# Kernel tuning notes

Measured on AMD Instinct MI355X. Metric: run time of the kernel, lower is better.

## Reference

```python
import jax, jax.numpy as jnp
import numpy as np

H = 50   # hidden_dim (hardcoded in module)
D = 16   # input_dim
B = 4096
T = 512

def _uniform(key, shape, k):
    return jax.random.uniform(key, shape, jnp.float32, -k, k)

def setup_inputs() -> dict:
    key = jax.random.key(0)
    ks = jax.random.split(key, 12)
    k = 1.0 / np.sqrt(H)  # PyTorch LSTM/Linear init bound
    return {
        "x": jax.random.normal(ks[0], (B, T, D), jnp.float32),
        "W_ih0": _uniform(ks[1], (4 * H, D), k),
        "W_hh0": _uniform(ks[2], (4 * H, H), k),
        "b_ih0": _uniform(ks[3], (4 * H,), k),
        "b_hh0": _uniform(ks[4], (4 * H,), k),
        "W_ih1": _uniform(ks[5], (4 * H, H), k),
        "W_hh1": _uniform(ks[6], (4 * H, H), k),
        "b_ih1": _uniform(ks[7], (4 * H,), k),
        "b_hh1": _uniform(ks[8], (4 * H,), k),
        "W_fc": _uniform(ks[9], (1, H), k),
        "b_fc": _uniform(ks[10], (1,), k),
    }

def _lstm_layer(x_tbd, W_ih, W_hh, b):
    # x_tbd: [T, B, Din]; returns (ys [T,B,H], h_final [B,H])
    Bsz = x_tbd.shape[1]
    # precompute input projections for all timesteps: [T, B, 4H]
    xproj = jnp.einsum('tbd,gd->tbg', x_tbd, W_ih) + b

    def step(carry, xp):
        h, c = carry
        gates = xp + h @ W_hh.T  # [B, 4H]
        i, f, g, o = jnp.split(gates, 4, axis=-1)  # torch gate order i,f,g,o
        i = jax.nn.sigmoid(i)
        f = jax.nn.sigmoid(f)
        g = jnp.tanh(g)
        o = jax.nn.sigmoid(o)
        c = f * c + i * g
        h = o * jnp.tanh(c)
        return (h, c), h

    init = (jnp.zeros((Bsz, H), x_tbd.dtype), jnp.zeros((Bsz, H), x_tbd.dtype))
    (h_fin, _), ys = jax.lax.scan(step, init, xproj)
    return ys, h_fin

def reference(x, W_ih0, W_hh0, b_ih0, b_hh0, W_ih1, W_hh1, b_ih1, b_hh1, W_fc, b_fc):
    x_tbd = jnp.transpose(x, (1, 0, 2))  # [T, B, D]
    ys0, _ = _lstm_layer(x_tbd, W_ih0, W_hh0, b_ih0 + b_hh0)
    _, h_n = _lstm_layer(ys0, W_ih1, W_hh1, b_ih1 + b_hh1)
    return h_n @ W_fc.T + b_fc  # [B, 1]
```

## Files before the change

### kernel.cpp

```cpp
#include <hip/hip_runtime.h>


#define TSTEPS 512
#define DIN 16
#define HID 50
#define BPB 16

typedef _Float16 half8 __attribute__((ext_vector_type(8)));
typedef _Float16 half4v __attribute__((ext_vector_type(4)));
typedef float f32x4 __attribute__((ext_vector_type(4)));

#define MF(A, B, C) __builtin_amdgcn_mfma_f32_16x16x32_f16((A), (B), (C), 0, 0, 0)

#define HBUF 2304
#define XBUF 1280
#define H0_O 0
#define H1_O 4608
#define X_O  9216
#define SH_BYTES (9216 + 4 * XBUF)

#define BAR() asm volatile("s_waitcnt lgkmcnt(0)\ns_barrier" ::: "memory")

__device__ __forceinline__ unsigned pack2h(float a, float b) {
  union { _Float16 h[2]; unsigned u; } pk;
  pk.h[0] = (_Float16)a;
  pk.h[1] = (_Float16)b;
  return pk.u;
}

__device__ __forceinline__ void cell2(const f32x4 gA, const f32x4 gB,
                                      float& cA, float& cB, float& hA, float& hB) {
  const float L2E = 1.4426950408889634f;
  float eiA = __builtin_amdgcn_exp2f(-L2E * gA[0]);
  float efA = __builtin_amdgcn_exp2f(-L2E * gA[1]);
  float egA = __builtin_amdgcn_exp2f(fminf(2.f * L2E * gA[2], 40.f));
  float eoA = __builtin_amdgcn_exp2f(-L2E * gA[3]);
  float eiB = __builtin_amdgcn_exp2f(-L2E * gB[0]);
  float efB = __builtin_amdgcn_exp2f(-L2E * gB[1]);
  float egB = __builtin_amdgcn_exp2f(fminf(2.f * L2E * gB[2], 40.f));
  float eoB = __builtin_amdgcn_exp2f(-L2E * gB[3]);
  float aA = 1.f + eiA, fA = 1.f + efA, bA = 1.f + egA;
  float aB = 1.f + eiB, fB = 1.f + efB, bB = 1.f + egB;
  float abA = aA * bA, abB = aB * bB;
  float tA = fmaf(egA - 1.f, fA, cA * abA);
  float tB = fmaf(egB - 1.f, fB, cB * abB);
  cA = tA * __builtin_amdgcn_rcpf(fA * abA);
  cB = tB * __builtin_amdgcn_rcpf(fB * abB);
  float ecA = __builtin_amdgcn_exp2f(fminf(2.f * L2E * cA, 40.f));
  float ecB = __builtin_amdgcn_exp2f(fminf(2.f * L2E * cB, 40.f));
  float qA = (1.f + eoA) * (1.f + ecA);
  float qB = (1.f + eoB) * (1.f + ecB);
  float r2 = __builtin_amdgcn_rcpf(qA * qB);
  hA = (ecA - 1.f) * (r2 * qB);
  hB = (ecB - 1.f) * (r2 * qA);
}

__device__ __forceinline__ half8 load_wfrag(const float* __restrict__ W, int kld,
                                            bool permk, int kreal, int gt, int kt,
                                            int lane) {
  const int gp = 16 * gt + (lane & 15);
  const int u = gp >> 2, j = gp & 3;
  const int kb = kt * 32 + (lane >> 4) * 8;
  half8 f;
#pragma unroll
  for (int i = 0; i < 8; ++i) {
    const int p = kb + i;
    const int kk = permk ? ((p & ~7) + (((p & 1) << 2) | ((p >> 1) & 3))) : p;
    float v = (u < HID && kk < kreal) ? W[(j * HID + u) * kld + kk] : 0.f;
    f[i] = (_Float16)v;
  }
  return f;
}

extern "C" __global__ void __launch_bounds__(512, 2)
lstm2_v8(const float* __restrict__ x,
         const float* __restrict__ Wih0, const float* __restrict__ Whh0,
         const float* __restrict__ bih0, const float* __restrict__ bhh0,
         const float* __restrict__ Wih1, const float* __restrict__ Whh1,
         const float* __restrict__ bih1, const float* __restrict__ bhh1,
         const float* __restrict__ Wfc, const float* __restrict__ bfc,
         float* __restrict__ out) {
  __shared__ __align__(16) char sh[SH_BYTES];
  const int tid = threadIdx.x;
  const int lane = tid & 63;
  const int wv = tid >> 6;
  const int bcol = lane & 15;
  const int kg = lane >> 4;
  const int bbase = blockIdx.x * BPB;
  const bool comp = (wv < 7);

  const int sbb = lane >> 2, q = lane & 3;
  const float* xrow = x + ((size_t)(bbase + sbb) * TSTEPS) * DIN + q * 4;

  for (int i = tid; i < SH_BYTES / 4; i += 512) ((int*)sh)[i] = 0;

  half8 w0x[2], w0h[2][2], w1i[2][2], w1h[2][2];
  f32x4 bias0v[2] = {{0,0,0,0},{0,0,0,0}}, bias1v[2] = {{0,0,0,0},{0,0,0,0}};
  if (comp) {
#pragma unroll
    for (int gi = 0; gi < 2; ++gi) {
      const int gt = 2 * wv + gi;
      w0x[gi] = load_wfrag(Wih0, DIN, false, DIN, gt, 0, lane);
#pragma unroll
      for (int kt = 0; kt < 2; ++kt) {
        w0h[gi][kt] = load_wfrag(Whh0, HID, true, HID, gt, kt, lane);
        w1i[gi][kt] = load_wfrag(Wih1, HID, true, HID, gt, kt, lane);
        w1h[gi][kt] = load_wfrag(Whh1, HID, true, HID, gt, kt, lane);
      }
      const int u = 8 * wv + 4 * gi + kg;
      if (u < HID) {
#pragma unroll
        for (int j = 0; j < 4; ++j) {
          bias0v[gi][j] = bih0[j * HID + u] + bhh0[j * HID + u];
          bias1v[gi][j] = bih1[j * HID + u] + bhh1[j * HID + u];
        }
      }
    }
  }
  float c0[2] = {0.f, 0.f}, c1[2] = {0.f, 0.f};
  const int hoff = bcol * 144 + kg * 16;
  const int xoff = bcol * 80 + kg * 16;
  const int wo32 = bcol * 144 + wv * 16 + kg * 4;

  BAR();

  if (wv == 7) {
#pragma unroll
    for (int t = 0; t < 3; ++t) {
      float4 xq = *(const float4*)(xrow + (size_t)t * DIN);
      half4v h4;
#pragma unroll
      for (int i = 0; i < 4; ++i) h4[i] = (_Float16)((const float*)&xq)[i];
      *(half4v*)(sh + X_O + t * XBUF + sbb * 80 + q * 8) = h4;
    }
  }
  BAR();

  float4 xrA, xrB;
  half8 bxc;
  if (comp) {
    half8 bx0 = *(const half8*)(sh + X_O + 0 * XBUF + xoff);
    bxc = *(const half8*)(sh + X_O + 1 * XBUF + xoff);
    f32x4 a0 = MF(w0x[0], bx0, bias0v[0]);
    f32x4 a1 = MF(w0x[1], bx0, bias0v[1]);
    float h0a, h0b;
    cell2(a0, a1, c0[0], c0[1], h0a, h0b);
    *(unsigned*)(sh + H0_O + wo32) = pack2h(h0a, h0b);
  } else if (wv == 7) {
    xrA = *(const float4*)(xrow + (size_t)3 * DIN);
    xrB = *(const float4*)(xrow + (size_t)4 * DIN);
  }
  BAR();

#define STEPCOMP(P, XSN)                                                       \
  do {                                                                         \
    half8 bh0[2], bh1[2];                                                      \
    _Pragma("unroll") for (int kt = 0; kt < 2; ++kt) {                         \
      bh0[kt] = *(const half8*)(sh + H0_O + (P)*HBUF + hoff + kt * 64);        \
      bh1[kt] = *(const half8*)(sh + H1_O + (P)*HBUF + hoff + kt * 64);        \
    }                                                                          \
    half8 bxn = *(const half8*)(sh + X_O + (XSN)*XBUF + xoff);                 \
    float h1n[2], h0n[2];                                                      \
    _Pragma("unroll") for (int gi = 0; gi < 2; ++gi) {                         \
      f32x4 qv = MF(w1i[gi][0], bh0[0], bias1v[gi]);                           \
      qv = MF(w1h[gi][0], bh1[0], qv);                                         \
      qv = MF(w1i[gi][1], bh0[1], qv);                                         \
      qv = MF(w1h[gi][1], bh1[1], qv);                                         \
      f32x4 rv = MF(w0x[gi], bxc, bias0v[gi]);                                 \
      rv = MF(w0h[gi][0], bh0[0], rv);                                         \
      rv = MF(w0h[gi][1], bh0[1], rv);                                         \
      cell2(qv, rv, c1[gi], c0[gi], h1n[gi], h0n[gi]);                         \
    }                                                                          \
    *(unsigned*)(sh + H1_O + ((P) ^ 1) * HBUF + wo32) = pack2h(h1n[0], h1n[1]);\
    *(unsigned*)(sh + H0_O + ((P) ^ 1) * HBUF + wo32) = pack2h(h0n[0], h0n[1]);\
    bxc = bxn;                                                                 \
  } while (0)

#define STEPX(T, SLOT, XR)                                                     \
  do {                                                                         \
    half4v h4;                                                                 \
    _Pragma("unroll") for (int i = 0; i < 4; ++i)                              \
        h4[i] = (_Float16)((const float*)&(XR))[i];                            \
    *(half4v*)(sh + X_O + (SLOT)*XBUF + sbb * 80 + q * 8) = h4;                \
    int tl = (T) + 5;                                                          \
    if (tl > TSTEPS - 1) tl = TSTEPS - 1;                                      \
    (XR) = *(const float4*)(xrow + (size_t)tl * DIN);                          \
  } while (0)

  for (int s = 0; s < TSTEPS; s += 4) {
    if (comp) { STEPCOMP(0, 2); } else if (wv == 7) { STEPX(s, 3, xrA); }
    BAR();
    if (comp) { STEPCOMP(1, 3); } else if (wv == 7) { STEPX(s + 1, 0, xrB); }
    BAR();
    if (comp) { STEPCOMP(0, 0); } else if (wv == 7) { STEPX(s + 2, 1, xrA); }
    BAR();
    if (comp) { STEPCOMP(1, 1); } else if (wv == 7) { STEPX(s + 3, 2, xrB); }
    BAR();
  }

  if (tid < BPB) {
    float acc = bfc[0];
#pragma unroll 10
    for (int u = 0; u < HID; ++u) {
      const int pp = (u & ~7) + 2 * (u & 3) + ((u >> 2) & 1);
      float h = (float)(*(const _Float16*)(sh + H1_O + tid * 144 + pp * 2));
      acc = fmaf(Wfc[u], h, acc);
    }
    out[bbase + tid] = acc;
  }
}

extern "C" void kernel_launch(void* const* d_in, const int* in_sizes, int n_in,
                              void* d_out, int out_size, void* d_ws, size_t ws_size,
                              hipStream_t stream) {
  (void)in_sizes; (void)n_in; (void)d_ws; (void)ws_size; (void)out_size;
  lstm2_v8<<<dim3(4096 / BPB), dim3(512), 0, stream>>>(
      (const float*)d_in[0], (const float*)d_in[1], (const float*)d_in[2],
      (const float*)d_in[3], (const float*)d_in[4], (const float*)d_in[5],
      (const float*)d_in[6], (const float*)d_in[7], (const float*)d_in[8],
      (const float*)d_in[9], (const float*)d_in[10], (float*)d_out);
}
```

Before: 398.1 us.

## Fold exp2 scaling constants into weights/bias, pack cell math, reorder MFMA chains

Premultiplies the gate weights and biases by -log2(e) (or 2*log2(e) for the g gate) so the cell no longer multiplies before each exp2. The cell state is kept pre-scaled by 2*log2(e), which removes the multiply before the tanh(c) exponent. The cell math is rewritten over 2-wide float vectors to allow packed FP32 ops, and h is packed with cvt_pkrtz. The MFMA chains for the two gate tiles are interleaved, and the layer-0 cell is computed and stored before layer 1 to hide MFMA latency. The trade-off is different fp16 rounding of the scaled weights, round-toward-zero conversion, and changed clamping.

```diff
diff --git a/kernel.cpp b/kernel.cpp
--- a/kernel.cpp
+++ b/kernel.cpp
@@ -8,7 +8,9 @@
 
 typedef _Float16 half8 __attribute__((ext_vector_type(8)));
 typedef _Float16 half4v __attribute__((ext_vector_type(4)));
+typedef __fp16 fp16x2 __attribute__((ext_vector_type(2)));
 typedef float f32x4 __attribute__((ext_vector_type(4)));
+typedef float f32x2 __attribute__((ext_vector_type(2)));
 
 #define MF(A, B, C) __builtin_amdgcn_mfma_f32_16x16x32_f16((A), (B), (C), 0, 0, 0)
 
@@ -21,43 +23,49 @@
 
 #define BAR() asm volatile("s_waitcnt lgkmcnt(0)\ns_barrier" ::: "memory")
 
+#define NL2E  (-1.4426950408889634f)
+#define P2L2E (2.8853900817779268f)
+
 __device__ __forceinline__ unsigned pack2h(float a, float b) {
-  union { _Float16 h[2]; unsigned u; } pk;
-  pk.h[0] = (_Float16)a;
-  pk.h[1] = (_Float16)b;
+  union { fp16x2 h; unsigned u; } pk;
+  pk.h = __builtin_amdgcn_cvt_pkrtz(a, b);
   return pk.u;
 }
 
-__device__ __forceinline__ void cell2(const f32x4 gA, const f32x4 gB,
-                                      float& cA, float& cB, float& hA, float& hB) {
-  const float L2E = 1.4426950408889634f;
-  float eiA = __builtin_amdgcn_exp2f(-L2E * gA[0]);
-  float efA = __builtin_amdgcn_exp2f(-L2E * gA[1]);
-  float egA = __builtin_amdgcn_exp2f(fminf(2.f * L2E * gA[2], 40.f));
-  float eoA = __builtin_amdgcn_exp2f(-L2E * gA[3]);
-  float eiB = __builtin_amdgcn_exp2f(-L2E * gB[0]);
-  float efB = __builtin_amdgcn_exp2f(-L2E * gB[1]);
-  float egB = __builtin_amdgcn_exp2f(fminf(2.f * L2E * gB[2], 40.f));
-  float eoB = __builtin_amdgcn_exp2f(-L2E * gB[3]);
-  float aA = 1.f + eiA, fA = 1.f + efA, bA = 1.f + egA;
-  float aB = 1.f + eiB, fB = 1.f + efB, bB = 1.f + egB;
-  float abA = aA * bA, abB = aB * bB;
-  float tA = fmaf(egA - 1.f, fA, cA * abA);
-  float tB = fmaf(egB - 1.f, fB, cB * abB);
-  cA = tA * __builtin_amdgcn_rcpf(fA * abA);
-  cB = tB * __builtin_amdgcn_rcpf(fB * abB);
-  float ecA = __builtin_amdgcn_exp2f(fminf(2.f * L2E * cA, 40.f));
-  float ecB = __builtin_amdgcn_exp2f(fminf(2.f * L2E * cB, 40.f));
-  float qA = (1.f + eoA) * (1.f + ecA);
-  float qB = (1.f + eoB) * (1.f + ecB);
-  float r2 = __builtin_amdgcn_rcpf(qA * qB);
-  hA = (ecA - 1.f) * (r2 * qB);
-  hB = (ecB - 1.f) * (r2 * qA);
+__device__ __forceinline__ f32x2 cell2p(const f32x4 gA, const f32x4 gB, f32x2& C) {
+  f32x2 gi = {gA[0], gB[0]}, gf = {gA[1], gB[1]};
+  f32x2 gg = {gA[2], gB[2]}, go = {gA[3], gB[3]};
+  f32x2 ei, ef, eg, eo;
+  ei[0] = __builtin_amdgcn_exp2f(gi[0]); ei[1] = __builtin_amdgcn_exp2f(gi[1]);
+  ef[0] = __builtin_amdgcn_exp2f(gf[0]); ef[1] = __builtin_amdgcn_exp2f(gf[1]);
+  eg[0] = __builtin_amdgcn_exp2f(gg[0]); eg[1] = __builtin_amdgcn_exp2f(gg[1]);
+  eo[0] = __builtin_amdgcn_exp2f(fminf(go[0], 30.f));
+  eo[1] = __builtin_amdgcn_exp2f(fminf(go[1], 30.f));
+  const f32x2 one = {1.f, 1.f};
+  const f32x2 c2 = {P2L2E, P2L2E};
+  f32x2 a = one + ei, f = one + ef, b = one + eg;
+  f32x2 ab = a * b;
+  f32x2 f2 = ef * c2 + c2;
+  f32x2 t = (eg - one) * f2 + C * ab;
+  f32x2 p = f * ab;
+  f32x2 rp;
+  rp[0] = __builtin_amdgcn_rcpf(p[0]);
+  rp[1] = __builtin_amdgcn_rcpf(p[1]);
+  C = t * rp;
+  f32x2 ec;
+  ec[0] = __builtin_amdgcn_exp2f(fminf(C[0], 30.f));
+  ec[1] = __builtin_amdgcn_exp2f(fminf(C[1], 30.f));
+  f32x2 q = (one + eo) * (one + ec);
+  float r2 = __builtin_amdgcn_rcpf(q[0] * q[1]);
+  f32x2 h;
+  h[0] = (ec[0] - 1.f) * (r2 * q[1]);
+  h[1] = (ec[1] - 1.f) * (r2 * q[0]);
+  return h;
 }
 
 __device__ __forceinline__ half8 load_wfrag(const float* __restrict__ W, int kld,
                                             bool permk, int kreal, int gt, int kt,
-                                            int lane) {
+                                            int lane, float scale) {
   const int gp = 16 * gt + (lane & 15);
   const int u = gp >> 2, j = gp & 3;
   const int kb = kt * 32 + (lane >> 4) * 8;
@@ -67,19 +75,19 @@
     const int p = kb + i;
     const int kk = permk ? ((p & ~7) + (((p & 1) << 2) | ((p >> 1) & 3))) : p;
     float v = (u < HID && kk < kreal) ? W[(j * HID + u) * kld + kk] : 0.f;
-    f[i] = (_Float16)v;
+    f[i] = (_Float16)(v * scale);
   }
   return f;
 }
 
 extern "C" __global__ void __launch_bounds__(512, 2)
-lstm2_v8(const float* __restrict__ x,
-         const float* __restrict__ Wih0, const float* __restrict__ Whh0,
-         const float* __restrict__ bih0, const float* __restrict__ bhh0,
-         const float* __restrict__ Wih1, const float* __restrict__ Whh1,
-         const float* __restrict__ bih1, const float* __restrict__ bhh1,
-         const float* __restrict__ Wfc, const float* __restrict__ bfc,
-         float* __restrict__ out) {
+lstm2_v10(const float* __restrict__ x,
+          const float* __restrict__ Wih0, const float* __restrict__ Whh0,
+          const float* __restrict__ bih0, const float* __restrict__ bhh0,
+          const float* __restrict__ Wih1, const float* __restrict__ Whh1,
+          const float* __restrict__ bih1, const float* __restrict__ bhh1,
+          const float* __restrict__ Wfc, const float* __restrict__ bfc,
+          float* __restrict__ out) {
   __shared__ __align__(16) char sh[SH_BYTES];
   const int tid = threadIdx.x;
   const int lane = tid & 63;
@@ -94,30 +102,32 @@
 
   for (int i = tid; i < SH_BYTES / 4; i += 512) ((int*)sh)[i] = 0;
 
+  const float wsc = ((lane & 3) == 2) ? P2L2E : NL2E;
   half8 w0x[2], w0h[2][2], w1i[2][2], w1h[2][2];
   f32x4 bias0v[2] = {{0,0,0,0},{0,0,0,0}}, bias1v[2] = {{0,0,0,0},{0,0,0,0}};
   if (comp) {
 #pragma unroll
     for (int gi = 0; gi < 2; ++gi) {
       const int gt = 2 * wv + gi;
-      w0x[gi] = load_wfrag(Wih0, DIN, false, DIN, gt, 0, lane);
+      w0x[gi] = load_wfrag(Wih0, DIN, false, DIN, gt, 0, lane, wsc);
 #pragma unroll
       for (int kt = 0; kt < 2; ++kt) {
-        w0h[gi][kt] = load_wfrag(Whh0, HID, true, HID, gt, kt, lane);
-        w1i[gi][kt] = load_wfrag(Wih1, HID, true, HID, gt, kt, lane);
-        w1h[gi][kt] = load_wfrag(Whh1, HID, true, HID, gt, kt, lane);
+        w0h[gi][kt] = load_wfrag(Whh0, HID, true, HID, gt, kt, lane, wsc);
+        w1i[gi][kt] = load_wfrag(Wih1, HID, true, HID, gt, kt, lane, wsc);
+        w1h[gi][kt] = load_wfrag(Whh1, HID, true, HID, gt, kt, lane, wsc);
       }
       const int u = 8 * wv + 4 * gi + kg;
       if (u < HID) {
 #pragma unroll
         for (int j = 0; j < 4; ++j) {
-          bias0v[gi][j] = bih0[j * HID + u] + bhh0[j * HID + u];
-          bias1v[gi][j] = bih1[j * HID + u] + bhh1[j * HID + u];
+          const float bs = (j == 2) ? P2L2E : NL2E;
+          bias0v[gi][j] = bs * (bih0[j * HID + u] + bhh0[j * HID + u]);
+          bias1v[gi][j] = bs * (bih1[j * HID + u] + bhh1[j * HID + u]);
         }
       }
     }
   }
-  float c0[2] = {0.f, 0.f}, c1[2] = {0.f, 0.f};
+  f32x2 C0 = {0.f, 0.f}, C1 = {0.f, 0.f};
   const int hoff = bcol * 144 + kg * 16;
   const int xoff = bcol * 80 + kg * 16;
   const int wo32 = bcol * 144 + wv * 16 + kg * 4;
@@ -143,9 +153,8 @@
     bxc = *(const half8*)(sh + X_O + 1 * XBUF + xoff);
     f32x4 a0 = MF(w0x[0], bx0, bias0v[0]);
     f32x4 a1 = MF(w0x[1], bx0, bias0v[1]);
-    float h0a, h0b;
-    cell2(a0, a1, c0[0], c0[1], h0a, h0b);
-    *(unsigned*)(sh + H0_O + wo32) = pack2h(h0a, h0b);
+    f32x2 H0 = cell2p(a0, a1, C0);
+    *(unsigned*)(sh + H0_O + wo32) = pack2h(H0[0], H0[1]);
   } else if (wv == 7) {
     xrA = *(const float4*)(xrow + (size_t)3 * DIN);
     xrB = *(const float4*)(xrow + (size_t)4 * DIN);
@@ -160,19 +169,24 @@
       bh1[kt] = *(const half8*)(sh + H1_O + (P)*HBUF + hoff + kt * 64);        \
     }                                                                          \
     half8 bxn = *(const half8*)(sh + X_O + (XSN)*XBUF + xoff);                 \
-    float h1n[2], h0n[2];                                                      \
-    _Pragma("unroll") for (int gi = 0; gi < 2; ++gi) {                         \
-      f32x4 qv = MF(w1i[gi][0], bh0[0], bias1v[gi]);                           \
-      qv = MF(w1h[gi][0], bh1[0], qv);                                         \
-      qv = MF(w1i[gi][1], bh0[1], qv);                                         \
-      qv = MF(w1h[gi][1], bh1[1], qv);                                         \
-      f32x4 rv = MF(w0x[gi], bxc, bias0v[gi]);                                 \
-      rv = MF(w0h[gi][0], bh0[0], rv);                                         \
-      rv = MF(w0h[gi][1], bh0[1], rv);                                         \
-      cell2(qv, rv, c1[gi], c0[gi], h1n[gi], h0n[gi]);                         \
-    }                                                                          \
-    *(unsigned*)(sh + H1_O + ((P) ^ 1) * HBUF + wo32) = pack2h(h1n[0], h1n[1]);\
-    *(unsigned*)(sh + H0_O + ((P) ^ 1) * HBUF + wo32) = pack2h(h0n[0], h0n[1]);\
+    f32x4 rv0 = MF(w0x[0], bxc, bias0v[0]);                                    \
+    f32x4 rv1 = MF(w0x[1], bxc, bias0v[1]);                                    \
+    rv0 = MF(w0h[0][0], bh0[0], rv0);                                          \
+    rv1 = MF(w0h[1][0], bh0[0], rv1);                                          \
+    rv0 = MF(w0h[0][1], bh0[1], rv0);                                          \
+    rv1 = MF(w0h[1][1], bh0[1], rv1);                                          \
+    f32x4 qv0 = MF(w1i[0][0], bh0[0], bias1v[0]);                              \
+    f32x4 qv1 = MF(w1i[1][0], bh0[0], bias1v[1]);                              \
+    qv0 = MF(w1h[0][0], bh1[0], qv0);                                          \
+    qv1 = MF(w1h[1][0], bh1[0], qv1);                                          \
+    qv0 = MF(w1i[0][1], bh0[1], qv0);                                          \
+    qv1 = MF(w1i[1][1], bh0[1], qv1);                                          \
+    qv0 = MF(w1h[0][1], bh1[1], qv0);                                          \
+    qv1 = MF(w1h[1][1], bh1[1], qv1);                                          \
+    f32x2 H0 = cell2p(rv0, rv1, C0);                                           \
+    *(unsigned*)(sh + H0_O + ((P) ^ 1) * HBUF + wo32) = pack2h(H0[0], H0[1]);  \
+    f32x2 H1 = cell2p(qv0, qv1, C1);                                           \
+    *(unsigned*)(sh + H1_O + ((P) ^ 1) * HBUF + wo32) = pack2h(H1[0], H1[1]);  \
     bxc = bxn;                                                                 \
   } while (0)
 
@@ -214,7 +228,7 @@
                               void* d_out, int out_size, void* d_ws, size_t ws_size,
                               hipStream_t stream) {
   (void)in_sizes; (void)n_in; (void)d_ws; (void)ws_size; (void)out_size;
-  lstm2_v8<<<dim3(4096 / BPB), dim3(512), 0, stream>>>(
+  lstm2_v10<<<dim3(4096 / BPB), dim3(512), 0, stream>>>(
       (const float*)d_in[0], (const float*)d_in[1], (const float*)d_in[2],
       (const float*)d_in[3], (const float*)d_in[4], (const float*)d_in[5],
       (const float*)d_in[6], (const float*)d_in[7], (const float*)d_in[8],
```

After: 330.7 us. 16.9% less time.
